# Kernel optimization log

Hardware: AMD Instinct MI355X
Metric: run time of the kernel (lower is better)

Reference implementation:

```python
import jax, jax.numpy as jnp
import numpy as np

NX = 65536   # spatial cells
T = 32       # time points
H = 128      # MLP hidden width
DX = 1.0     # spatial resolution (init kwarg dx)
S0, S1 = -1.0, 1.0  # fixed stencil (learn_stencil=False)


def setup_inputs() -> dict:
    key = jax.random.key(0)
    k1, k2, k3, k4 = jax.random.split(key, 4)
    t = jnp.arange(T, dtype=jnp.float32) * 0.01          # time grid, dt=0.01
    u0 = jax.random.uniform(k1, (NX,), jnp.float32)      # initial state
    inv_sqrt_h = jnp.float32(1.0 / np.sqrt(H))
    W1 = jax.random.normal(k2, (1, H), jnp.float32)
    W2 = jax.random.normal(k3, (H, H), jnp.float32) * inv_sqrt_h
    W3 = jax.random.normal(k4, (H, 1), jnp.float32) * inv_sqrt_h
    D = jnp.full((1,), 0.01, jnp.float32)                # diffusion coefficient
    BC = jnp.zeros((2, 1), jnp.float32)                  # Dirichlet BC values
    return {"t": t, "u0": u0, "W1": W1, "W2": W2, "W3": W3, "D": D, "BC": BC}


def _flux(u, W1, W2, W3, D, BC):
    # per-cell MLP (func_nn): Linear->Tanh->Linear->Tanh->Linear, no bias, no sigmoid
    h = jnp.tanh(u[:, None] @ W1)        # [Nx, H]
    h = jnp.tanh(h @ W2)                 # [Nx, H]
    a = (h @ W3)[:, 0]                   # [Nx]
    a_plus = jax.nn.relu(a)
    a_min = -jax.nn.relu(-a)
    d = D[0]
    # left fluxes
    lb = d * (S0 * u[0] + S1 * BC[0, 0]) - a_plus[0] / DX * (-S0 * u[0] - S1 * BC[0, 0])
    ln = d * (S0 * u[1:] + S1 * u[:-1]) - a_plus[1:] / DX * (-S0 * u[1:] - S1 * u[:-1])
    left = jnp.concatenate([lb[None], ln])
    # right fluxes
    rb = d * (S0 * u[-1] + S1 * BC[1, 0]) - a_min[-1] / DX * (S0 * u[-1] + S1 * BC[1, 0])
    rn = d * (S0 * u[:-1] + S1 * u[1:]) - a_min[:-1] / DX * (S0 * u[:-1] + S1 * u[1:])
    right = jnp.concatenate([rn, rb[None]])
    return left + right


def reference(t, u0, W1, W2, W3, D, BC):
    # Neural-ODE integration of du/dt = flux_kernel(u); fixed-step RK4 over grid t
    f = lambda u: _flux(u, W1, W2, W3, D, BC)

    def step(u, dt):
        k1 = f(u)
        k2 = f(u + 0.5 * dt * k1)
        k3 = f(u + 0.5 * dt * k2)
        k4 = f(u + dt * k3)
        un = u + (dt / 6.0) * (k1 + 2.0 * k2 + 2.0 * k3 + k4)
        return un, un

    _, us = jax.lax.scan(step, u0, jnp.diff(t))
    return jnp.concatenate([u0[None], us], axis=0)  # [T, Nx]
```

## Files before the change

### kernel.cpp

```cpp
#include <hip/hip_runtime.h>

#define NXC 65536
#define TT 32
#define HH 128
#define TABN 6145
#define TABNP 6146
#define TABLO (-1.0f)
#define TABINV 2048.0f
#define OUTW 64
#define VC 3
#define WINW 192
#define HALO 64

typedef __attribute__((ext_vector_type(8))) short bf16x8;
typedef __attribute__((ext_vector_type(4))) float f32x4;
typedef unsigned short u16;

__device__ __forceinline__ float bf2f(u16 b) {
    union { unsigned int u; float f; } v; v.u = ((unsigned int)b) << 16; return v.f;
}
__device__ __forceinline__ u16 f2bf(float f) {
    union { float f; unsigned int u; } v; v.f = f;
    return (u16)((v.u + 0x7fffu + ((v.u >> 16) & 1u)) >> 16);
}
__device__ __forceinline__ bool is_bf16_mode(const void* t) {
    return ((const u16*)t)[1] != 0;
}

#if __has_builtin(__builtin_amdgcn_exp2f)
#define EXP2F(x) __builtin_amdgcn_exp2f(x)
#else
#define EXP2F(x) exp2f(x)
#endif
#if __has_builtin(__builtin_amdgcn_rcpf)
#define RCPF(x) __builtin_amdgcn_rcpf(x)
#else
#define RCPF(x) (1.0f / (x))
#endif

__device__ __forceinline__ float fast_tanh(float x) {
    float e = EXP2F(x * 2.8853900817779268f);
    return 1.0f - 2.0f * RCPF(e + 1.0f);
}

__global__ void w2swz_kernel(const void* t, const void* W2,
                             u16* __restrict__ w2frag) {
    bool bf = is_bf16_mode(t);
    int i = blockIdx.x * 256 + threadIdx.x;
    int j = i & 7;
    int lane = (i >> 3) & 63;
    int ks = (i >> 9) & 3;
    int nt = i >> 11;
    int k = ks * 32 + (lane >> 4) * 8 + j;
    int n = nt * 16 + (lane & 15);
    w2frag[i] = bf ? ((const u16*)W2)[k * HH + n]
                   : f2bf(((const float*)W2)[k * HH + n]);
}

__global__ __launch_bounds__(256) void tabbuild_kernel(
    const void* traw, const void* W1, const void* W3,
    const u16* __restrict__ w2frag, float* __restrict__ atab) {
    __shared__ float w1s[HH];
    __shared__ float w3s[HH];
    bool bf = is_bf16_mode(traw);
    int tid = threadIdx.x;
    if (tid < HH)
        w1s[tid] = bf ? bf2f(((const u16*)W1)[tid]) : ((const float*)W1)[tid];
    else
        w3s[tid - HH] = bf ? bf2f(((const u16*)W3)[tid - HH])
                           : ((const float*)W3)[tid - HH];
    __syncthreads();

    int lane = tid & 63;
    int wave = tid >> 6;
    int q = lane >> 4;
    int m = lane & 15;
    int base = (blockIdx.x * 4 + wave) * 16;
    float uin = TABLO + (float)(base + m) * (1.0f / TABINV);

    bf16x8 afrag[4];
#pragma unroll
    for (int ks = 0; ks < 4; ++ks)
#pragma unroll
        for (int j = 0; j < 8; ++j) {
            float h = fast_tanh(uin * w1s[ks * 32 + q * 8 + j]);
            afrag[ks][j] = (short)f2bf(h);
        }

    const bf16x8* w2f = (const bf16x8*)w2frag;
    float p0 = 0.f, p1 = 0.f, p2 = 0.f, p3 = 0.f;
#pragma unroll
    for (int nt = 0; nt < 8; ++nt) {
        f32x4 acc = {0.f, 0.f, 0.f, 0.f};
#pragma unroll
        for (int ks = 0; ks < 4; ++ks) {
            bf16x8 b = w2f[(nt * 4 + ks) * 64 + lane];
            acc = __builtin_amdgcn_mfma_f32_16x16x32_bf16(afrag[ks], b, acc, 0, 0, 0);
        }
        float w3v = w3s[nt * 16 + m];
        p0 += fast_tanh(acc[0]) * w3v;
        p1 += fast_tanh(acc[1]) * w3v;
        p2 += fast_tanh(acc[2]) * w3v;
        p3 += fast_tanh(acc[3]) * w3v;
    }
#pragma unroll
    for (int sh = 1; sh < 16; sh <<= 1) {
        p0 += __shfl_xor(p0, sh, 64);
        p1 += __shfl_xor(p1, sh, 64);
        p2 += __shfl_xor(p2, sh, 64);
        p3 += __shfl_xor(p3, sh, 64);
    }
    int r = m & 3;
    float a = (r == 0) ? p0 : (r == 1) ? p1 : (r == 2) ? p2 : p3;
    if (m < 4) {
        int e = base + q * 4 + r;
        if (e < TABNP) atab[e] = a;
    }
}

__global__ __launch_bounds__(256) void chunk_kernel(
    const void* traw, const void* uin, float* __restrict__ uout,
    const void* Draw, const void* BCraw, const float* __restrict__ atab,
    void* __restrict__ outbase, int s0, int nsteps) {
    __shared__ __align__(16) float tabs[TABNP + 2];
    __shared__ float t32s[TT];

    int tid = threadIdx.x;
    bool bf = is_bf16_mode(traw);

    for (int e = tid * 4; e < TABNP + 2; e += 1024)
        *(float4*)(tabs + e) = *(const float4*)(atab + e);
    if (tid < TT)
        t32s[tid] = bf ? bf2f(((const u16*)traw)[tid]) : ((const float*)traw)[tid];

    float d   = bf ? bf2f(((const u16*)Draw)[0])  : ((const float*)Draw)[0];
    float bc0 = bf ? bf2f(((const u16*)BCraw)[0]) : ((const float*)BCraw)[0];
    float bc1 = bf ? bf2f(((const u16*)BCraw)[1]) : ((const float*)BCraw)[1];

    int lane = tid & 63;
    int wid = blockIdx.x * 4 + (tid >> 6);
    int gb = wid * OUTW - HALO + lane * VC;
    int i0 = lane * VC;
    bool first = (s0 == 0);

    float v[VC], ub[VC];
    bool gok[VC], own[VC];
#pragma unroll
    for (int j = 0; j < VC; ++j) {
        int g = gb + j;
        int i = i0 + j;
        gok[j] = (g >= 0) && (g < NXC);
        own[j] = (i >= HALO) && (i < HALO + OUTW);
        float x;
        if (first) {
            if (bf) {
                u16 raw = gok[j] ? ((const u16*)uin)[g] : (u16)0;
                x = bf2f(raw);
                if (own[j]) ((u16*)outbase)[g] = raw;
            } else {
                float raw = gok[j] ? ((const float*)uin)[g] : 0.f;
                x = raw;
                if (own[j]) ((float*)outbase)[g] = raw;
            }
        } else {
            x = gok[j] ? ((const float*)uin)[g] : 0.f;
        }
        if (!gok[j]) x = (g < 0) ? bc0 : bc1;
        v[j] = x;
        ub[j] = x;
    }
    __syncthreads();

    for (int st = 0; st < nsteps; ++st) {
        int step = s0 + st;
        float dt = t32s[step + 1] - t32s[step];
        float dt2 = 0.5f * dt, dt6 = dt * (1.0f / 6.0f);
        float kacc[VC], kv[VC];
#pragma unroll
        for (int j = 0; j < VC; ++j) kacc[j] = 0.f;
#pragma unroll
        for (int s = 0; s < 4; ++s) {
            float cnext = (s < 2) ? dt2 : dt;
            float wgt = (s == 1 || s == 2) ? 2.f : 1.f;
            float vup = __shfl_up(v[VC - 1], 1, 64);
            float vdn = __shfl_down(v[0], 1, 64);
#pragma unroll
            for (int j = 0; j < VC; ++j) {
                float vc = v[j];
                float vl = (j == 0) ? vup : v[j - 1];
                float vr = (j == VC - 1) ? vdn : v[j + 1];
                float f = fmaf(vc, TABINV, (-TABLO) * TABINV);
                f = fminf(fmaxf(f, 0.0f), (float)(TABN - 1));
                int e0 = (int)f;
                float frac = f - (float)e0;
                float t0 = tabs[e0];
                float t1 = tabs[e0 + 1];
                float a = fmaf(frac, t1 - t0, t0);
                float ap = fmaxf(a, 0.f);
                float am = fminf(a, 0.f);
                kv[j] = (vl - vc) * (d + ap) + (vr - vc) * (d - am);
            }
#pragma unroll
            for (int j = 0; j < VC; ++j) {
                kacc[j] += wgt * kv[j];
                float nv = (s < 3) ? fmaf(cnext, kv[j], ub[j])
                                   : fmaf(dt6, kacc[j], ub[j]);
                if (gok[j]) {
                    v[j] = nv;
                    if (s == 3) ub[j] = nv;
                }
            }
        }
        if (bf) {
            u16* orow = (u16*)outbase + (size_t)(step + 1) * NXC;
#pragma unroll
            for (int j = 0; j < VC; ++j)
                if (own[j]) orow[gb + j] = f2bf(ub[j]);
        } else {
            float* orow = (float*)outbase + (size_t)(step + 1) * NXC;
#pragma unroll
            for (int j = 0; j < VC; ++j)
                if (own[j]) orow[gb + j] = ub[j];
        }
    }
    if (uout != nullptr) {
#pragma unroll
        for (int j = 0; j < VC; ++j)
            if (own[j]) uout[gb + j] = ub[j];
    }
}

extern "C" void kernel_launch(void* const* d_in, const int* in_sizes, int n_in,
                              void* d_out, int out_size, void* d_ws,
                              size_t ws_size, hipStream_t stream) {
    const void* t  = d_in[0];
    const void* u0 = d_in[1];
    const void* W1 = d_in[2];
    const void* W2 = d_in[3];
    const void* W3 = d_in[4];
    const void* Dp = d_in[5];
    const void* BC = d_in[6];

    float* atab = (float*)d_ws;
    u16* w2frag = (u16*)(atab + TABNP + 2);
    float* uB = (float*)(w2frag + 16384);

    w2swz_kernel<<<64, 256, 0, stream>>>(t, W2, w2frag);
    tabbuild_kernel<<<(TABNP + 63) / 64, 256, 0, stream>>>(t, W1, W3, w2frag, atab);

    chunk_kernel<<<256, 256, 0, stream>>>(t, u0, uB, Dp, BC, atab, d_out, 0, 16);
    chunk_kernel<<<256, 256, 0, stream>>>(t, uB, nullptr, Dp, BC, atab, d_out, 16, 15);
}
```

Before: 100.6 us.

## Fuse two time-chunk launches into one block-wide overlapping-window integration kernel

Replaces the two chunk_kernel launches (16 and 15 steps with per-wave 64-cell output windows) with a single launch that integrates all 31 steps. Each 256-thread block now covers a 512-cell window, 2 cells per thread, with a 224-cell halo, and passes edge values between waves through shared memory with a __syncthreads per RK stage. This removes the second launch, the intermediate state buffer and the per-wave halo redundancy. In exchange it uses 1024 blocks each loading the full lookup table into LDS, adds 124 block barriers per block, and writes outputs with paired stores.

```diff
diff --git a/kernel.cpp b/kernel.cpp
--- a/kernel.cpp
+++ b/kernel.cpp
@@ -7,10 +7,10 @@
 #define TABNP 6146
 #define TABLO (-1.0f)
 #define TABINV 2048.0f
-#define OUTW 64
-#define VC 3
-#define WINW 192
-#define HALO 64
+#define OUTB 64
+#define WINB 512
+#define HALOB 224
+#define NSTEPS 31
 
 typedef __attribute__((ext_vector_type(8))) short bf16x8;
 typedef __attribute__((ext_vector_type(4))) float f32x4;
@@ -118,12 +118,13 @@
     }
 }
 
-__global__ __launch_bounds__(256) void chunk_kernel(
-    const void* traw, const void* uin, float* __restrict__ uout,
-    const void* Draw, const void* BCraw, const float* __restrict__ atab,
-    void* __restrict__ outbase, int s0, int nsteps) {
+__global__ __launch_bounds__(256) void integrate_kernel(
+    const void* traw, const void* u0, const void* Draw, const void* BCraw,
+    const float* __restrict__ atab, void* __restrict__ outbase) {
     __shared__ __align__(16) float tabs[TABNP + 2];
     __shared__ float t32s[TT];
+    __shared__ float eL[2][4];
+    __shared__ float eR[2][4];
 
     int tid = threadIdx.x;
     bool bf = is_bf16_mode(traw);
@@ -138,57 +139,60 @@
     float bc1 = bf ? bf2f(((const u16*)BCraw)[1]) : ((const float*)BCraw)[1];
 
     int lane = tid & 63;
-    int wid = blockIdx.x * 4 + (tid >> 6);
-    int gb = wid * OUTW - HALO + lane * VC;
-    int i0 = lane * VC;
-    bool first = (s0 == 0);
-
-    float v[VC], ub[VC];
-    bool gok[VC], own[VC];
-#pragma unroll
-    for (int j = 0; j < VC; ++j) {
+    int w = tid >> 6;
+    int gb = blockIdx.x * OUTB - HALOB + tid * 2;
+    bool own = (tid >= HALOB / 2) && (tid < (HALOB + OUTB) / 2);
+
+    float v[2], ub[2];
+    bool gok[2];
+#pragma unroll
+    for (int j = 0; j < 2; ++j) {
         int g = gb + j;
-        int i = i0 + j;
         gok[j] = (g >= 0) && (g < NXC);
-        own[j] = (i >= HALO) && (i < HALO + OUTW);
         float x;
-        if (first) {
-            if (bf) {
-                u16 raw = gok[j] ? ((const u16*)uin)[g] : (u16)0;
-                x = bf2f(raw);
-                if (own[j]) ((u16*)outbase)[g] = raw;
-            } else {
-                float raw = gok[j] ? ((const float*)uin)[g] : 0.f;
-                x = raw;
-                if (own[j]) ((float*)outbase)[g] = raw;
-            }
+        if (bf) {
+            u16 raw = gok[j] ? ((const u16*)u0)[g] : (u16)0;
+            x = bf2f(raw);
         } else {
-            x = gok[j] ? ((const float*)uin)[g] : 0.f;
+            x = gok[j] ? ((const float*)u0)[g] : 0.f;
         }
         if (!gok[j]) x = (g < 0) ? bc0 : bc1;
         v[j] = x;
         ub[j] = x;
     }
+    if (own) {
+        if (bf) {
+            unsigned int pk = (unsigned int)f2bf(ub[0])
+                            | ((unsigned int)f2bf(ub[1]) << 16);
+            *(unsigned int*)&((u16*)outbase)[gb] = pk;
+        } else {
+            *(float2*)&((float*)outbase)[gb] = make_float2(ub[0], ub[1]);
+        }
+    }
     __syncthreads();
 
-    for (int st = 0; st < nsteps; ++st) {
-        int step = s0 + st;
-        float dt = t32s[step + 1] - t32s[step];
+    for (int st = 0; st < NSTEPS; ++st) {
+        float dt = t32s[st + 1] - t32s[st];
         float dt2 = 0.5f * dt, dt6 = dt * (1.0f / 6.0f);
-        float kacc[VC], kv[VC];
-#pragma unroll
-        for (int j = 0; j < VC; ++j) kacc[j] = 0.f;
+        float kacc[2] = {0.f, 0.f};
 #pragma unroll
         for (int s = 0; s < 4; ++s) {
+            int p = s & 1;
             float cnext = (s < 2) ? dt2 : dt;
             float wgt = (s == 1 || s == 2) ? 2.f : 1.f;
-            float vup = __shfl_up(v[VC - 1], 1, 64);
+            if (lane == 63) eR[p][w] = v[1];
+            if (lane == 0)  eL[p][w] = v[0];
+            __syncthreads();
+            float vup = __shfl_up(v[1], 1, 64);
             float vdn = __shfl_down(v[0], 1, 64);
-#pragma unroll
-            for (int j = 0; j < VC; ++j) {
+            if (lane == 0)  vup = (w > 0) ? eR[p][w - 1] : v[0];
+            if (lane == 63) vdn = (w < 3) ? eL[p][w + 1] : v[1];
+            float kv[2];
+#pragma unroll
+            for (int j = 0; j < 2; ++j) {
                 float vc = v[j];
-                float vl = (j == 0) ? vup : v[j - 1];
-                float vr = (j == VC - 1) ? vdn : v[j + 1];
+                float vl = (j == 0) ? vup : v[0];
+                float vr = (j == 0) ? v[1] : vdn;
                 float f = fmaf(vc, TABINV, (-TABLO) * TABINV);
                 f = fminf(fmaxf(f, 0.0f), (float)(TABN - 1));
                 int e0 = (int)f;
@@ -201,7 +205,7 @@
                 kv[j] = (vl - vc) * (d + ap) + (vr - vc) * (d - am);
             }
 #pragma unroll
-            for (int j = 0; j < VC; ++j) {
+            for (int j = 0; j < 2; ++j) {
                 kacc[j] += wgt * kv[j];
                 float nv = (s < 3) ? fmaf(cnext, kv[j], ub[j])
                                    : fmaf(dt6, kacc[j], ub[j]);
@@ -211,22 +215,16 @@
                 }
             }
         }
-        if (bf) {
-            u16* orow = (u16*)outbase + (size_t)(step + 1) * NXC;
-#pragma unroll
-            for (int j = 0; j < VC; ++j)
-                if (own[j]) orow[gb + j] = f2bf(ub[j]);
-        } else {
-            float* orow = (float*)outbase + (size_t)(step + 1) * NXC;
-#pragma unroll
-            for (int j = 0; j < VC; ++j)
-                if (own[j]) orow[gb + j] = ub[j];
-        }
-    }
-    if (uout != nullptr) {
-#pragma unroll
-        for (int j = 0; j < VC; ++j)
-            if (own[j]) uout[gb + j] = ub[j];
+        if (own) {
+            size_t rb = (size_t)(st + 1) * NXC + gb;
+            if (bf) {
+                unsigned int pk = (unsigned int)f2bf(ub[0])
+                                | ((unsigned int)f2bf(ub[1]) << 16);
+                *(unsigned int*)&((u16*)outbase)[rb] = pk;
+            } else {
+                *(float2*)&((float*)outbase)[rb] = make_float2(ub[0], ub[1]);
+            }
+        }
     }
 }
 
@@ -243,11 +241,8 @@
 
     float* atab = (float*)d_ws;
     u16* w2frag = (u16*)(atab + TABNP + 2);
-    float* uB = (float*)(w2frag + 16384);
 
     w2swz_kernel<<<64, 256, 0, stream>>>(t, W2, w2frag);
     tabbuild_kernel<<<(TABNP + 63) / 64, 256, 0, stream>>>(t, W1, W3, w2frag, atab);
-
-    chunk_kernel<<<256, 256, 0, stream>>>(t, u0, uB, Dp, BC, atab, d_out, 0, 16);
-    chunk_kernel<<<256, 256, 0, stream>>>(t, uB, nullptr, Dp, BC, atab, d_out, 16, 15);
-}
+    integrate_kernel<<<NXC / OUTB, 256, 0, stream>>>(t, u0, Dp, BC, atab, d_out);
+}
```

Result: slower. 128.4 us (+27.6%).
